# Performance work log

Hardware: AMD Instinct MI355X
Metric: run time of the kernel (lower is better)

The kernel has to match this reference:

```python
import jax, jax.numpy as jnp
import numpy as np

H = 512
B = 32
T = 2048


def setup_inputs() -> dict:
    key = jax.random.key(0)
    ks = jax.random.split(key, 8)
    hidden = jax.random.normal(ks[0], (1, B, H), dtype=jnp.float32)
    encoder_outputs = jax.random.normal(ks[1], (T, B, H), dtype=jnp.float32)
    coverage = jax.random.uniform(ks[2], (B, T), dtype=jnp.float32)
    # nn.Linear(3H, H): weight [H, 3H], bias [H]
    W_attn = jax.random.normal(ks[3], (H, 3 * H), dtype=jnp.float32) / np.sqrt(3 * H)
    b_attn = jax.random.normal(ks[4], (H,), dtype=jnp.float32) / np.sqrt(3 * H)
    # v ~ Normal(0, 1/sqrt(H))
    v = jax.random.normal(ks[5], (H,), dtype=jnp.float32) / np.sqrt(H)
    # nn.Linear(1, H, bias=False): weight [H, 1]
    W_cov = jax.random.normal(ks[6], (H, 1), dtype=jnp.float32)
    return {"hidden": hidden, "encoder_outputs": encoder_outputs, "coverage": coverage,
            "W_attn": W_attn, "b_attn": b_attn, "v": v, "W_cov": W_cov}


def reference(hidden, encoder_outputs, coverage, W_attn, b_attn, v, W_cov):
    # hidden: [1,B,H], encoder_outputs: [T,B,H], coverage: [B,T]
    enc = jnp.transpose(encoder_outputs, (1, 0, 2))          # [B,T,H]
    b, t, h = enc.shape
    hrep = jnp.broadcast_to(hidden[0][:, None, :], (b, t, h))  # [B,T,H]
    # coverage_feature = Linear(1,H,bias=False)(coverage[...,None]) -> outer product
    cov_feat = coverage[..., None] * W_cov[:, 0]               # [B,T,H]
    x = jnp.concatenate([hrep, enc, cov_feat], axis=-1)        # [B,T,3H]
    energy = jax.nn.relu(jnp.einsum('btk,hk->bth', x, W_attn) + b_attn)  # [B,T,H]
    scores = jnp.einsum('bth,h->bt', energy, v)                # [B,T]
    attn_weights = jax.nn.softmax(scores, axis=1)              # softmax over T
    coverage_new = coverage + attn_weights                     # [B,T]
    return attn_weights[:, None, :], coverage_new
```

## Files before the change

kernel.cpp:

```cpp
#include <hip/hip_runtime.h>
#include <hip/hip_bf16.h>

typedef unsigned short u16;
typedef unsigned int u32;
typedef __attribute__((ext_vector_type(8))) short bf16x8;
typedef __attribute__((ext_vector_type(4))) float f32x4;

#define T_DIM 2048
#define B_DIM 32
#define H_DIM 512
#define M_DIM (T_DIM * B_DIM)

__device__ inline unsigned pack2(float a, float b) {
  union { __hip_bfloat162 h2; unsigned u; } c;
  c.h2 = __float22bfloat162_rn(make_float2(a, b));
  return c.u;
}

__device__ __forceinline__ void gld16(const void* g, void* s) {
  __builtin_amdgcn_global_load_lds(
      (const __attribute__((address_space(1))) void*)g,
      (__attribute__((address_space(3))) void*)s, 16, 0, 0);
}

__global__ __launch_bounds__(256) void prep_kernel(
    const float* __restrict__ hidden, const float* __restrict__ W_attn,
    const float* __restrict__ b_attn, const float* __restrict__ W_cov,
    u16* __restrict__ W2bf, float* __restrict__ r, float* __restrict__ u)
{
  const int tid = blockIdx.x * 256 + threadIdx.x;
  const int pair = tid >> 2;
  const int kq = tid & 3;
  const int b = pair >> 9, h = pair & 511;

  {
    const float* hid = hidden + b * 512 + kq * 128;
    const float* w1 = W_attn + (size_t)h * 1536 + kq * 128;
    float acc = 0.f;
    #pragma unroll 8
    for (int k = 0; k < 128; k += 4) {
      float4 x = *(const float4*)(hid + k);
      float4 w = *(const float4*)(w1 + k);
      acc += x.x * w.x + x.y * w.y + x.z * w.z + x.w * w.w;
    }
    acc += __shfl_xor(acc, 1);
    acc += __shfl_xor(acc, 2);
    if (kq == 0) r[pair] = acc + b_attn[h];
  }

  {
    int j0 = tid * 4;
    int hh = j0 >> 9, kk = j0 & 511;
    float4 w = *(const float4*)(W_attn + (size_t)hh * 1536 + 512 + kk);
    uint2 p;
    p.x = pack2(w.x, w.y);
    p.y = pack2(w.z, w.w);
    int f = hh >> 4, c = hh & 15;
    int ks = kk >> 5, quad = (kk >> 3) & 3, e = kk & 7;
    *(uint2*)(W2bf + (size_t)((f * 16 + ks) * 64 + quad * 16 + c) * 8 + e) = p;
  }

  if (tid < 2048) {
    int h3 = tid >> 2;
    const float* w3 = W_attn + (size_t)h3 * 1536 + 1024 + kq * 128;
    const float* wc = W_cov + kq * 128;
    float su = 0.f;
    #pragma unroll 8
    for (int k = 0; k < 128; k += 4) {
      float4 a = *(const float4*)(w3 + k);
      float4 c = *(const float4*)(wc + k);
      su += a.x * c.x + a.y * c.y + a.z * c.z + a.w * c.w;
    }
    su += __shfl_xor(su, 1);
    su += __shfl_xor(su, 2);
    if (kq == 0) u[h3] = su;
  }
}

__global__ __launch_bounds__(512, 4) void gemm_score(
    const float* __restrict__ enc, const u16* __restrict__ W2bf,
    const float* __restrict__ r, const float* __restrict__ u,
    const float* __restrict__ vv, const float* __restrict__ cov,
    float* __restrict__ part)
{
  const int bid = blockIdx.x;
  const int t = (bid & 7) * 256 + (bid >> 3);
  const int m0 = t * 32;
  const int tid = threadIdx.x;
  const int lane = tid & 63;
  const int w = tid >> 6;
  const int quad = lane >> 4, col = lane & 15;

  __shared__ float As[32 * 512];

  #pragma unroll
  for (int q = 0; q < 8; ++q) {
    int n = w * 8 + q;
    int rr = n >> 1, hh = n & 1;
    int gsrc = hh * 64 + (lane ^ (rr & 7));
    gld16(enc + (size_t)(m0 + rr) * 512 + gsrc * 4, (void*)(As + n * 256));
  }
  __syncthreads();

  f32x4 acc[2][4] = {};
  const u16* bbase = W2bf + (size_t)w * 32768 + lane * 8;

  bf16x8 bb[2][4];
  #pragma unroll
  for (int j = 0; j < 4; ++j) {
    bb[0][j] = *(const bf16x8*)(bbase + j * 8192);
    bb[1][j] = *(const bf16x8*)(bbase + j * 8192 + 512);
  }

  const int o0 = (((quad * 2)    ) ^ (col & 7)) * 4;
  const int o1 = (((quad * 2) + 1) ^ (col & 7)) * 4;
  const float* arow0 = As + col * 512;

  float4 areg[2][2][2];
  #pragma unroll
  for (int i = 0; i < 2; ++i) {
    const float* ap = arow0 + i * 8192;
    areg[0][i][0] = *(const float4*)(ap + o0);
    areg[0][i][1] = *(const float4*)(ap + o1);
  }

  #pragma unroll
  for (int ks = 0; ks < 16; ++ks) {
    if (ks < 15) {
      #pragma unroll
      for (int i = 0; i < 2; ++i) {
        const float* ap = arow0 + i * 8192 + (ks + 1) * 32;
        areg[(ks + 1) & 1][i][0] = *(const float4*)(ap + o0);
        areg[(ks + 1) & 1][i][1] = *(const float4*)(ap + o1);
      }
    }
    #pragma unroll
    for (int i = 0; i < 2; ++i) {
      float4 f0 = areg[ks & 1][i][0];
      float4 f1 = areg[ks & 1][i][1];
      union { bf16x8 v; u32 uu[4]; } af;
      af.uu[0] = pack2(f0.x, f0.y);
      af.uu[1] = pack2(f0.z, f0.w);
      af.uu[2] = pack2(f1.x, f1.y);
      af.uu[3] = pack2(f1.z, f1.w);
      #pragma unroll
      for (int j = 0; j < 4; ++j)
        acc[i][j] = __builtin_amdgcn_mfma_f32_16x16x32_bf16(af.v, bb[ks & 1][j], acc[i][j], 0, 0, 0);
    }
    if (ks < 14) {
      #pragma unroll
      for (int j = 0; j < 4; ++j)
        bb[ks & 1][j] = *(const bf16x8*)(bbase + j * 8192 + (ks + 2) * 512);
    }
  }

  float uj[4], vj[4];
  #pragma unroll
  for (int j = 0; j < 4; ++j) {
    int gh = w * 64 + j * 16 + col;
    uj[j] = u[gh];
    vj[j] = vv[gh];
  }

  __syncthreads();
  float* red = As;

  #pragma unroll
  for (int i = 0; i < 2; ++i) {
    #pragma unroll
    for (int reg = 0; reg < 4; ++reg) {
      int b = i * 16 + quad * 4 + reg;
      float cv = cov[b * 2048 + t];
      float s = 0.f;
      #pragma unroll
      for (int j = 0; j < 4; ++j) {
        float rv = r[b * 512 + w * 64 + j * 16 + col];
        float e = acc[i][j][reg] + rv + cv * uj[j];
        e = fmaxf(e, 0.f);
        s += e * vj[j];
      }
      s += __shfl_xor(s, 1);
      s += __shfl_xor(s, 2);
      s += __shfl_xor(s, 4);
      s += __shfl_xor(s, 8);
      if (col == 0) red[w * 32 + b] = s;
    }
  }
  __syncthreads();
  if (tid < 32) {
    float s = 0.f;
    #pragma unroll
    for (int p = 0; p < 8; ++p) s += red[p * 32 + tid];
    part[(size_t)tid * 2048 + t] = s;
  }
}

__global__ __launch_bounds__(256) void softmax_kernel(
    const float* __restrict__ part, const float* __restrict__ cov, float* __restrict__ out)
{
  const int b = blockIdx.x;
  const int tid = threadIdx.x;
  const int lane = tid & 63, wid = tid >> 6;
  __shared__ float red[4];
  float loc[8];
  float lmax = -3.4e38f;
  #pragma unroll
  for (int i = 0; i < 8; ++i) {
    int t = tid + i * 256;
    float s = part[(size_t)b * 2048 + t];
    loc[i] = s;
    lmax = fmaxf(lmax, s);
  }
  #pragma unroll
  for (int o = 32; o; o >>= 1) lmax = fmaxf(lmax, __shfl_xor(lmax, o));
  if (lane == 0) red[wid] = lmax;
  __syncthreads();
  float bmax = fmaxf(fmaxf(red[0], red[1]), fmaxf(red[2], red[3]));
  __syncthreads();
  float lsum = 0.f;
  #pragma unroll
  for (int i = 0; i < 8; ++i) { loc[i] = __expf(loc[i] - bmax); lsum += loc[i]; }
  #pragma unroll
  for (int o = 32; o; o >>= 1) lsum += __shfl_xor(lsum, o);
  if (lane == 0) red[wid] = lsum;
  __syncthreads();
  float inv = 1.0f / (red[0] + red[1] + red[2] + red[3]);
  #pragma unroll
  for (int i = 0; i < 8; ++i) {
    int t = tid + i * 256;
    float a = loc[i] * inv;
    out[b * 2048 + t] = a;
    out[65536 + b * 2048 + t] = cov[b * 2048 + t] + a;
  }
}

extern "C" void kernel_launch(void* const* d_in, const int* in_sizes, int n_in,
                              void* d_out, int out_size, void* d_ws, size_t ws_size,
                              hipStream_t stream) {
  const float* hidden = (const float*)d_in[0];
  const float* enc    = (const float*)d_in[1];
  const float* cov    = (const float*)d_in[2];
  const float* W_attn = (const float*)d_in[3];
  const float* b_attn = (const float*)d_in[4];
  const float* vv     = (const float*)d_in[5];
  const float* W_cov  = (const float*)d_in[6];
  float* out = (float*)d_out;

  u16* W2bf = (u16*)d_ws;
  float* r  = (float*)((char*)d_ws + 512 * 1024);
  float* u  = r + 32 * 512;
  float* part = u + 512;

  hipLaunchKernelGGL(prep_kernel, dim3(256), dim3(256), 0, stream,
                     hidden, W_attn, b_attn, W_cov, W2bf, r, u);
  hipLaunchKernelGGL(gemm_score, dim3(2048), dim3(512), 0, stream,
                     enc, W2bf, r, u, vv, cov, part);
  hipLaunchKernelGGL(softmax_kernel, dim3(32), dim3(256), 0, stream,
                     part, cov, out);
}
```

Before: 267.4 us.

## Use 64-row tiles with 16 waves and double-buffered K-chunk LDS loads

Each block now computes 64 rows (two time steps) with 16 waves arranged as 2 row groups by 8 column groups, so every W2 fragment load from global/L2 serves twice as many rows. The encoder tile is streamed in four 128-wide K chunks into a double-buffered LDS buffer, overlapping the async global-to-LDS load of the next chunk with MFMA work on the current one. This is meant to halve B-operand traffic and hide the initial full-tile load latency, at the cost of extra barriers per chunk and larger 1024-thread blocks, which may limit occupancy. The removal of the bid-to-t interleaving also changes which time steps run concurrently.

After: 278.2 us. +4.0%, slower.

```diff
diff --git a/kernel.cpp b/kernel.cpp
--- a/kernel.cpp
+++ b/kernel.cpp
@@ -9,7 +9,6 @@
 #define T_DIM 2048
 #define B_DIM 32
 #define H_DIM 512
-#define M_DIM (T_DIM * B_DIM)
 
 __device__ inline unsigned pack2(float a, float b) {
   union { __hip_bfloat162 h2; unsigned u; } c;
@@ -77,34 +76,24 @@
   }
 }
 
-__global__ __launch_bounds__(512, 4) void gemm_score(
+__global__ __launch_bounds__(1024, 4) void gemm_score(
     const float* __restrict__ enc, const u16* __restrict__ W2bf,
     const float* __restrict__ r, const float* __restrict__ u,
     const float* __restrict__ vv, const float* __restrict__ cov,
     float* __restrict__ part)
 {
-  const int bid = blockIdx.x;
-  const int t = (bid & 7) * 256 + (bid >> 3);
-  const int m0 = t * 32;
+  const int tile = blockIdx.x;
+  const int m0 = tile * 64;
   const int tid = threadIdx.x;
   const int lane = tid & 63;
   const int w = tid >> 6;
+  const int wr = w >> 3;
+  const int wc = w & 7;
   const int quad = lane >> 4, col = lane & 15;
 
-  __shared__ float As[32 * 512];
-
-  #pragma unroll
-  for (int q = 0; q < 8; ++q) {
-    int n = w * 8 + q;
-    int rr = n >> 1, hh = n & 1;
-    int gsrc = hh * 64 + (lane ^ (rr & 7));
-    gld16(enc + (size_t)(m0 + rr) * 512 + gsrc * 4, (void*)(As + n * 256));
-  }
-  __syncthreads();
-
-  f32x4 acc[2][4] = {};
-  const u16* bbase = W2bf + (size_t)w * 32768 + lane * 8;
-
+  __shared__ float As[2][64 * 128];
+
+  const u16* bbase = W2bf + (size_t)wc * 32768 + lane * 8;
   bf16x8 bb[2][4];
   #pragma unroll
   for (int j = 0; j < 4; ++j) {
@@ -112,69 +101,98 @@
     bb[1][j] = *(const bf16x8*)(bbase + j * 8192 + 512);
   }
 
+  {
+    #pragma unroll
+    for (int q = 0; q < 2; ++q) {
+      int n = w * 2 + q;
+      int rr = n * 2 + (lane >> 5);
+      int gl = lane & 31;
+      int gsrc = gl ^ (rr & 7);
+      gld16(enc + (size_t)(m0 + rr) * 512 + gsrc * 4, (void*)(&As[0][n * 256]));
+    }
+  }
+  __syncthreads();
+
+  f32x4 acc[2][4] = {};
   const int o0 = (((quad * 2)    ) ^ (col & 7)) * 4;
   const int o1 = (((quad * 2) + 1) ^ (col & 7)) * 4;
-  const float* arow0 = As + col * 512;
 
   float4 areg[2][2][2];
-  #pragma unroll
-  for (int i = 0; i < 2; ++i) {
-    const float* ap = arow0 + i * 8192;
-    areg[0][i][0] = *(const float4*)(ap + o0);
-    areg[0][i][1] = *(const float4*)(ap + o1);
-  }
-
-  #pragma unroll
-  for (int ks = 0; ks < 16; ++ks) {
-    if (ks < 15) {
+
+  #pragma unroll
+  for (int kc = 0; kc < 4; ++kc) {
+    if (kc < 3) {
+      #pragma unroll
+      for (int q = 0; q < 2; ++q) {
+        int n = w * 2 + q;
+        int rr = n * 2 + (lane >> 5);
+        int gl = lane & 31;
+        int gsrc = gl ^ (rr & 7);
+        gld16(enc + (size_t)(m0 + rr) * 512 + (kc + 1) * 128 + gsrc * 4,
+              (void*)(&As[(kc + 1) & 1][n * 256]));
+      }
+    }
+    const float* abase = &As[kc & 1][0];
+    #pragma unroll
+    for (int i = 0; i < 2; ++i) {
+      const float* ap = abase + (wr * 32 + i * 16 + col) * 128;
+      areg[0][i][0] = *(const float4*)(ap + o0);
+      areg[0][i][1] = *(const float4*)(ap + o1);
+    }
+    #pragma unroll
+    for (int ksl = 0; ksl < 4; ++ksl) {
+      const int ks = kc * 4 + ksl;
+      if (ksl < 3) {
+        #pragma unroll
+        for (int i = 0; i < 2; ++i) {
+          const float* ap = abase + (wr * 32 + i * 16 + col) * 128 + (ksl + 1) * 32;
+          areg[(ksl + 1) & 1][i][0] = *(const float4*)(ap + o0);
+          areg[(ksl + 1) & 1][i][1] = *(const float4*)(ap + o1);
+        }
+      }
       #pragma unroll
       for (int i = 0; i < 2; ++i) {
-        const float* ap = arow0 + i * 8192 + (ks + 1) * 32;
-        areg[(ks + 1) & 1][i][0] = *(const float4*)(ap + o0);
-        areg[(ks + 1) & 1][i][1] = *(const float4*)(ap + o1);
-      }
-    }
-    #pragma unroll
-    for (int i = 0; i < 2; ++i) {
-      float4 f0 = areg[ks & 1][i][0];
-      float4 f1 = areg[ks & 1][i][1];
-      union { bf16x8 v; u32 uu[4]; } af;
-      af.uu[0] = pack2(f0.x, f0.y);
-      af.uu[1] = pack2(f0.z, f0.w);
-      af.uu[2] = pack2(f1.x, f1.y);
-      af.uu[3] = pack2(f1.z, f1.w);
-      #pragma unroll
-      for (int j = 0; j < 4; ++j)
-        acc[i][j] = __builtin_amdgcn_mfma_f32_16x16x32_bf16(af.v, bb[ks & 1][j], acc[i][j], 0, 0, 0);
-    }
-    if (ks < 14) {
-      #pragma unroll
-      for (int j = 0; j < 4; ++j)
-        bb[ks & 1][j] = *(const bf16x8*)(bbase + j * 8192 + (ks + 2) * 512);
-    }
+        float4 f0 = areg[ksl & 1][i][0];
+        float4 f1 = areg[ksl & 1][i][1];
+        union { bf16x8 v; u32 uu[4]; } af;
+        af.uu[0] = pack2(f0.x, f0.y);
+        af.uu[1] = pack2(f0.z, f0.w);
+        af.uu[2] = pack2(f1.x, f1.y);
+        af.uu[3] = pack2(f1.z, f1.w);
+        #pragma unroll
+        for (int j = 0; j < 4; ++j)
+          acc[i][j] = __builtin_amdgcn_mfma_f32_16x16x32_bf16(af.v, bb[ks & 1][j], acc[i][j], 0, 0, 0);
+      }
+      if (ks < 14) {
+        #pragma unroll
+        for (int j = 0; j < 4; ++j)
+          bb[ks & 1][j] = *(const bf16x8*)(bbase + j * 8192 + (ks + 2) * 512);
+      }
+    }
+    __syncthreads();
   }
 
   float uj[4], vj[4];
   #pragma unroll
   for (int j = 0; j < 4; ++j) {
-    int gh = w * 64 + j * 16 + col;
+    int gh = wc * 64 + j * 16 + col;
     uj[j] = u[gh];
     vj[j] = vv[gh];
   }
-
-  __syncthreads();
-  float* red = As;
+  float* red = &As[0][0];
 
   #pragma unroll
   for (int i = 0; i < 2; ++i) {
     #pragma unroll
     for (int reg = 0; reg < 4; ++reg) {
-      int b = i * 16 + quad * 4 + reg;
-      float cv = cov[b * 2048 + t];
+      int bl = i * 16 + quad * 4 + reg;
+      int rl = wr * 32 + bl;
+      int t = tile * 2 + wr;
+      float cv = cov[bl * 2048 + t];
       float s = 0.f;
       #pragma unroll
       for (int j = 0; j < 4; ++j) {
-        float rv = r[b * 512 + w * 64 + j * 16 + col];
+        float rv = r[bl * 512 + wc * 64 + j * 16 + col];
         float e = acc[i][j][reg] + rv + cv * uj[j];
         e = fmaxf(e, 0.f);
         s += e * vj[j];
@@ -183,15 +201,16 @@
       s += __shfl_xor(s, 2);
       s += __shfl_xor(s, 4);
       s += __shfl_xor(s, 8);
-      if (col == 0) red[w * 32 + b] = s;
-    }
-  }
-  __syncthreads();
-  if (tid < 32) {
+      if (col == 0) red[rl * 8 + wc] = s;
+    }
+  }
+  __syncthreads();
+  if (tid < 64) {
     float s = 0.f;
     #pragma unroll
-    for (int p = 0; p < 8; ++p) s += red[p * 32 + tid];
-    part[(size_t)tid * 2048 + t] = s;
+    for (int p = 0; p < 8; ++p) s += red[tid * 8 + p];
+    int t = tile * 2 + (tid >> 5), bl = tid & 31;
+    part[(size_t)bl * 2048 + t] = s;
   }
 }
 
@@ -253,7 +272,7 @@
 
   hipLaunchKernelGGL(prep_kernel, dim3(256), dim3(256), 0, stream,
                      hidden, W_attn, b_attn, W_cov, W2bf, r, u);
-  hipLaunchKernelGGL(gemm_score, dim3(2048), dim3(512), 0, stream,
+  hipLaunchKernelGGL(gemm_score, dim3(1024), dim3(1024), 0, stream,
                      enc, W2bf, r, u, vv, cov, part);
   hipLaunchKernelGGL(softmax_kernel, dim3(32), dim3(256), 0, stream,
                      part, cov, out);
```

## Process four T-rows per block with double-buffered bf16 LDS staging

Applied to the files above, without the earlier changes.

The GEMM-score kernel now runs on 512 blocks instead of 2048. Each block loops over four timesteps and prefetches the next timestep's encoder rows into registers while the MFMA work for the current one runs. The rows are converted to bf16 once and stored in swizzled double-buffered LDS, which replaces the fp32 LDS copy and the per-fragment conversion inside the MFMA loop. This removes the async global-to-LDS load and halves LDS footprint per buffer, but it lowers grid parallelism and re-streams the weight fragments from cache for each timestep.

Result: slower. 627.0 us (+134.5%).

```diff
diff --git a/kernel.cpp b/kernel.cpp
--- a/kernel.cpp
+++ b/kernel.cpp
@@ -9,18 +9,11 @@
 #define T_DIM 2048
 #define B_DIM 32
 #define H_DIM 512
-#define M_DIM (T_DIM * B_DIM)
 
 __device__ inline unsigned pack2(float a, float b) {
   union { __hip_bfloat162 h2; unsigned u; } c;
   c.h2 = __float22bfloat162_rn(make_float2(a, b));
   return c.u;
-}
-
-__device__ __forceinline__ void gld16(const void* g, void* s) {
-  __builtin_amdgcn_global_load_lds(
-      (const __attribute__((address_space(1))) void*)g,
-      (__attribute__((address_space(3))) void*)s, 16, 0, 0);
 }
 
 __global__ __launch_bounds__(256) void prep_kernel(
@@ -83,76 +76,41 @@
     const float* __restrict__ vv, const float* __restrict__ cov,
     float* __restrict__ part)
 {
-  const int bid = blockIdx.x;
-  const int t = (bid & 7) * 256 + (bid >> 3);
-  const int m0 = t * 32;
+  const int blk = blockIdx.x;
   const int tid = threadIdx.x;
   const int lane = tid & 63;
   const int w = tid >> 6;
   const int quad = lane >> 4, col = lane & 15;
 
-  __shared__ float As[32 * 512];
-
-  #pragma unroll
-  for (int q = 0; q < 8; ++q) {
-    int n = w * 8 + q;
-    int rr = n >> 1, hh = n & 1;
-    int gsrc = hh * 64 + (lane ^ (rr & 7));
-    gld16(enc + (size_t)(m0 + rr) * 512 + gsrc * 4, (void*)(As + n * 256));
-  }
-  __syncthreads();
-
-  f32x4 acc[2][4] = {};
+  __shared__ u16 As[2][32 * 512];
+  __shared__ float red[256];
+
   const u16* bbase = W2bf + (size_t)w * 32768 + lane * 8;
 
-  bf16x8 bb[2][4];
-  #pragma unroll
-  for (int j = 0; j < 4; ++j) {
-    bb[0][j] = *(const bf16x8*)(bbase + j * 8192);
-    bb[1][j] = *(const bf16x8*)(bbase + j * 8192 + 512);
-  }
-
-  const int o0 = (((quad * 2)    ) ^ (col & 7)) * 4;
-  const int o1 = (((quad * 2) + 1) ^ (col & 7)) * 4;
-  const float* arow0 = As + col * 512;
-
-  float4 areg[2][2][2];
-  #pragma unroll
-  for (int i = 0; i < 2; ++i) {
-    const float* ap = arow0 + i * 8192;
-    areg[0][i][0] = *(const float4*)(ap + o0);
-    areg[0][i][1] = *(const float4*)(ap + o1);
-  }
-
-  #pragma unroll
-  for (int ks = 0; ks < 16; ++ks) {
-    if (ks < 15) {
-      #pragma unroll
-      for (int i = 0; i < 2; ++i) {
-        const float* ap = arow0 + i * 8192 + (ks + 1) * 32;
-        areg[(ks + 1) & 1][i][0] = *(const float4*)(ap + o0);
-        areg[(ks + 1) & 1][i][1] = *(const float4*)(ap + o1);
-      }
-    }
-    #pragma unroll
-    for (int i = 0; i < 2; ++i) {
-      float4 f0 = areg[ks & 1][i][0];
-      float4 f1 = areg[ks & 1][i][1];
-      union { bf16x8 v; u32 uu[4]; } af;
-      af.uu[0] = pack2(f0.x, f0.y);
-      af.uu[1] = pack2(f0.z, f0.w);
-      af.uu[2] = pack2(f1.x, f1.y);
-      af.uu[3] = pack2(f1.z, f1.w);
-      #pragma unroll
-      for (int j = 0; j < 4; ++j)
-        acc[i][j] = __builtin_amdgcn_mfma_f32_16x16x32_bf16(af.v, bb[ks & 1][j], acc[i][j], 0, 0, 0);
-    }
-    if (ks < 14) {
-      #pragma unroll
-      for (int j = 0; j < 4; ++j)
-        bb[ks & 1][j] = *(const bf16x8*)(bbase + j * 8192 + (ks + 2) * 512);
-    }
-  }
+  const int srow = w * 4 + (lane >> 4);
+  const int g16 = lane & 15;
+
+  float4 sb[8];
+  {
+    const float* gb = enc + ((size_t)blk * 4 * 32 + srow) * 512;
+    #pragma unroll
+    for (int q = 0; q < 4; ++q) {
+      int G = g16 + 16 * q;
+      sb[q * 2]     = *(const float4*)(gb + G * 8);
+      sb[q * 2 + 1] = *(const float4*)(gb + G * 8 + 4);
+    }
+  }
+  #pragma unroll
+  for (int q = 0; q < 4; ++q) {
+    int G = g16 + 16 * q;
+    uint4 p;
+    p.x = pack2(sb[q * 2].x,     sb[q * 2].y);
+    p.y = pack2(sb[q * 2].z,     sb[q * 2].w);
+    p.z = pack2(sb[q * 2 + 1].x, sb[q * 2 + 1].y);
+    p.w = pack2(sb[q * 2 + 1].z, sb[q * 2 + 1].w);
+    *(uint4*)&As[0][srow * 512 + (G ^ (srow & 7)) * 8] = p;
+  }
+  __syncthreads();
 
   float uj[4], vj[4];
   #pragma unroll
@@ -162,36 +120,88 @@
     vj[j] = vv[gh];
   }
 
-  __syncthreads();
-  float* red = As;
-
-  #pragma unroll
-  for (int i = 0; i < 2; ++i) {
-    #pragma unroll
-    for (int reg = 0; reg < 4; ++reg) {
-      int b = i * 16 + quad * 4 + reg;
-      float cv = cov[b * 2048 + t];
+  #pragma unroll 1
+  for (int tl = 0; tl < 4; ++tl) {
+    const int t = blk * 4 + tl;
+    const int cur = tl & 1;
+
+    if (tl < 3) {
+      const float* gb = enc + ((size_t)(t + 1) * 32 + srow) * 512;
+      #pragma unroll
+      for (int q = 0; q < 4; ++q) {
+        int G = g16 + 16 * q;
+        sb[q * 2]     = *(const float4*)(gb + G * 8);
+        sb[q * 2 + 1] = *(const float4*)(gb + G * 8 + 4);
+      }
+    }
+    __builtin_amdgcn_sched_barrier(0);
+
+    bf16x8 bb[2][4];
+    #pragma unroll
+    for (int j = 0; j < 4; ++j) {
+      bb[0][j] = *(const bf16x8*)(bbase + j * 8192);
+      bb[1][j] = *(const bf16x8*)(bbase + j * 8192 + 512);
+    }
+    f32x4 acc[2][4] = {};
+    #pragma unroll
+    for (int ks = 0; ks < 16; ++ks) {
+      #pragma unroll
+      for (int i = 0; i < 2; ++i) {
+        int row = i * 16 + col;
+        bf16x8 af = *(const bf16x8*)&As[cur][row * 512 + ((ks * 4 + quad) ^ (col & 7)) * 8];
+        #pragma unroll
+        for (int j = 0; j < 4; ++j)
+          acc[i][j] = __builtin_amdgcn_mfma_f32_16x16x32_bf16(af, bb[ks & 1][j], acc[i][j], 0, 0, 0);
+      }
+      if (ks < 14) {
+        #pragma unroll
+        for (int j = 0; j < 4; ++j)
+          bb[ks & 1][j] = *(const bf16x8*)(bbase + j * 8192 + (ks + 2) * 512);
+      }
+    }
+
+    #pragma unroll
+    for (int i = 0; i < 2; ++i) {
+      #pragma unroll
+      for (int reg = 0; reg < 4; ++reg) {
+        int bl = i * 16 + quad * 4 + reg;
+        float cv = cov[bl * 2048 + t];
+        float s = 0.f;
+        #pragma unroll
+        for (int j = 0; j < 4; ++j) {
+          float rv = r[bl * 512 + w * 64 + j * 16 + col];
+          float e = acc[i][j][reg] + rv + cv * uj[j];
+          e = fmaxf(e, 0.f);
+          s += e * vj[j];
+        }
+        s += __shfl_xor(s, 1);
+        s += __shfl_xor(s, 2);
+        s += __shfl_xor(s, 4);
+        s += __shfl_xor(s, 8);
+        if (col == 0) red[w * 32 + bl] = s;
+      }
+    }
+    __syncthreads();
+    if (tid < 32) {
       float s = 0.f;
       #pragma unroll
-      for (int j = 0; j < 4; ++j) {
-        float rv = r[b * 512 + w * 64 + j * 16 + col];
-        float e = acc[i][j][reg] + rv + cv * uj[j];
-        e = fmaxf(e, 0.f);
-        s += e * vj[j];
-      }
-      s += __shfl_xor(s, 1);
-      s += __shfl_xor(s, 2);
-      s += __shfl_xor(s, 4);
-      s += __shfl_xor(s, 8);
-      if (col == 0) red[w * 32 + b] = s;
-    }
-  }
-  __syncthreads();
-  if (tid < 32) {
-    float s = 0.f;
-    #pragma unroll
-    for (int p = 0; p < 8; ++p) s += red[p * 32 + tid];
-    part[(size_t)tid * 2048 + t] = s;
+      for (int p = 0; p < 8; ++p) s += red[p * 32 + tid];
+      part[(size_t)tid * 2048 + t] = s;
+    }
+
+    if (tl < 3) {
+      #pragma unroll
+      for (int q = 0; q < 4; ++q) {
+        int G = g16 + 16 * q;
+        uint4 p;
+        p.x = pack2(sb[q * 2].x,     sb[q * 2].y);
+        p.y = pack2(sb[q * 2].z,     sb[q * 2].w);
+        p.z = pack2(sb[q * 2 + 1].x, sb[q * 2 + 1].y);
+        p.w = pack2(sb[q * 2 + 1].z, sb[q * 2 + 1].w);
+        *(uint4*)&As[cur ^ 1][srow * 512 + (G ^ (srow & 7)) * 8] = p;
+      }
+    }
+    __syncthreads();
   }
 }
 
@@ -253,7 +263,7 @@
 
   hipLaunchKernelGGL(prep_kernel, dim3(256), dim3(256), 0, stream,
                      hidden, W_attn, b_attn, W_cov, W2bf, r, u);
-  hipLaunchKernelGGL(gemm_score, dim3(2048), dim3(512), 0, stream,
+  hipLaunchKernelGGL(gemm_score, dim3(512), dim3(512), 0, stream,
                      enc, W2bf, r, u, vv, cov, part);
   hipLaunchKernelGGL(softmax_kernel, dim3(32), dim3(256), 0, stream,
                      part, cov, out);
```
